# Performance work log

Hardware: AMD Instinct MI355X
Metric: run time of the kernel (lower is better)

The kernel has to match this reference:

```python
import jax, jax.numpy as jnp
import numpy as np

INDIM = 1024
OUTDIM = 2048
BATCH = 8192


def _kaiming_uniform(key, shape):
    # torch kaiming_uniform_ default: a=sqrt(5) -> gain=sqrt(2/(1+5))=sqrt(1/3),
    # fan_in = shape[0] (first dim for 2D), bound = gain*sqrt(3/fan_in) = 1/sqrt(fan_in)
    fan_in = shape[0]
    bound = 1.0 / np.sqrt(fan_in)
    return jax.random.uniform(key, shape, dtype=jnp.float32, minval=-bound, maxval=bound)


def setup_inputs() -> dict:
    key = jax.random.key(0)
    kx, kp = jax.random.split(key)
    x = jax.random.normal(kx, (BATCH, INDIM), dtype=jnp.float32)
    prototypes = _kaiming_uniform(kp, (INDIM, OUTDIM))
    return {"x": x, "prototypes": prototypes}


def reference(x, prototypes):
    # score[b, o] = -sum_i (x[b,i] - P[i,o])^2
    #             = -(||x_b||^2 - 2 x_b . P_:,o + ||P_:,o||^2)
    x_sq = jnp.sum(x * x, axis=1, keepdims=True)          # [B, 1]
    p_sq = jnp.sum(prototypes * prototypes, axis=0)       # [O]
    cross = jnp.matmul(x, prototypes)                      # [B, O] GEMM
    return 2.0 * cross - x_sq - p_sq[None, :]
```

## Files before the change

### kernel.cpp

```cpp
#include <hip/hip_runtime.h>
#include <hip/hip_bf16.h>
#include <cstdint>

#define BATCH  8192
#define INDIM  1024
#define OUTDIM 2048

typedef float  f32x4   __attribute__((ext_vector_type(4)));
typedef float  f32x16  __attribute__((ext_vector_type(16)));
typedef int    i32x2   __attribute__((ext_vector_type(2)));
typedef int    i32x4   __attribute__((ext_vector_type(4)));
typedef int    i32x8   __attribute__((ext_vector_type(8)));

__device__ __forceinline__ uint32_t pk_fp8x4(float a, float b, float c, float d) {
    uint32_t v = 0;
    v = __builtin_amdgcn_cvt_pk_fp8_f32(a, b, v, false);
    v = __builtin_amdgcn_cvt_pk_fp8_f32(c, d, v, true);
    return v;
}

__device__ __forceinline__ void async_copy16(const void* g, void* l) {
    __builtin_amdgcn_global_load_lds(
        (__attribute__((address_space(1))) void*)(g),
        (__attribute__((address_space(3))) void*)(l),
        16, 0, 0);
}

__device__ __forceinline__ int k4(int r) { return (r ^ (r >> 2)) & 3; }

__global__ __launch_bounds__(256) void prep_x(const float* __restrict__ x,
                                              uint8_t* __restrict__ xq8,
                                              float* __restrict__ xsq) {
    const int wave = threadIdx.x >> 6;
    const int lane = threadIdx.x & 63;
    const int row  = blockIdx.x * 4 + wave;
    const f32x4* src = (const f32x4*)(x + (size_t)row * INDIM);
    uint32_t* dst = (uint32_t*)(xq8 + (size_t)row * INDIM);
    float s = 0.f;
#pragma unroll
    for (int w = 0; w < 4; ++w) {
        const f32x4 v = src[lane + w * 64];
        s += v.x * v.x + v.y * v.y + v.z * v.z + v.w * v.w;
        dst[lane + w * 64] = pk_fp8x4(v.x, v.y, v.z, v.w);
    }
#pragma unroll
    for (int off = 32; off > 0; off >>= 1) s += __shfl_down(s, off);
    if (lane == 0) xsq[row] = s;
}

__global__ __launch_bounds__(256) void prep_p(const float* __restrict__ P,
                                              uint8_t* __restrict__ pt8,
                                              float* __restrict__ psq_part) {
    __shared__ float tile[64][33];
    __shared__ float psums[32];
    const int tid = threadIdx.x;
    const int o0  = blockIdx.x * 32;
    const int k0  = blockIdx.y * 256;
    const int kk  = tid >> 3;
    const int oq  = tid & 7;
    const int so  = tid >> 3;
    const int skc = (tid & 7) * 8;
    float a4[4] = {0.f, 0.f, 0.f, 0.f};
    if (tid < 32) psums[tid] = 0.f;
    for (int st = 0; st < 4; ++st) {
        __syncthreads();
#pragma unroll
        for (int r2 = 0; r2 < 2; ++r2) {
            const int k = r2 * 32 + kk;
            const float4 v = *(const float4*)(P + (size_t)(k0 + st * 64 + k) * OUTDIM + o0 + oq * 4);
            tile[k][oq * 4 + 0] = v.x;
            tile[k][oq * 4 + 1] = v.y;
            tile[k][oq * 4 + 2] = v.z;
            tile[k][oq * 4 + 3] = v.w;
            a4[0] += v.x * v.x; a4[1] += v.y * v.y;
            a4[2] += v.z * v.z; a4[3] += v.w * v.w;
        }
        __syncthreads();
        i32x2 w;
        w.x = pk_fp8x4(tile[skc + 0][so] * 32.f, tile[skc + 1][so] * 32.f,
                       tile[skc + 2][so] * 32.f, tile[skc + 3][so] * 32.f);
        w.y = pk_fp8x4(tile[skc + 4][so] * 32.f, tile[skc + 5][so] * 32.f,
                       tile[skc + 6][so] * 32.f, tile[skc + 7][so] * 32.f);
        *(i32x2*)(pt8 + (size_t)(o0 + so) * INDIM + k0 + st * 64 + skc) = w;
    }
#pragma unroll
    for (int e = 0; e < 4; ++e) atomicAdd(&psums[oq * 4 + e], a4[e]);
    __syncthreads();
    if (tid < 32) psq_part[(size_t)blockIdx.y * OUTDIM + o0 + tid] = psums[tid];
}

#define TM 256
#define TN 256
#define BKB 64

__global__ __launch_bounds__(512, 2) void gemm_ep(const uint8_t* __restrict__ xq8,
                                                  const uint8_t* __restrict__ pt8,
                                                  const float* __restrict__ xsq,
                                                  const float* __restrict__ psq_part,
                                                  float* __restrict__ out) {
    __shared__ __align__(16) uint8_t As[2][TM * BKB];
    __shared__ __align__(16) uint8_t Bs[2][TN * BKB];

    const int tid  = threadIdx.x;
    const int nb   = blockIdx.x & 7;
    const int mb   = blockIdx.x >> 3;
    const int m0   = mb * TM;
    const int n0   = nb * TN;
    const int wave = tid >> 6;
    const int lane = tid & 63;
    const int wm   = (wave >> 2) * 128;
    const int wn   = (wave & 3) * 64;
    const int l31  = lane & 31;
    const int half = lane >> 5;

    const int sr0 = tid >> 2;
    const int sq0 = (tid & 3) ^ k4(sr0);
    const int sr1 = sr0 + 128;
    const int sq1 = (tid & 3) ^ k4(sr1);

    f32x16 acc[4][2];
#pragma unroll
    for (int i = 0; i < 4; ++i)
#pragma unroll
        for (int j = 0; j < 2; ++j)
#pragma unroll
            for (int e = 0; e < 16; ++e) acc[i][j][e] = 0.f;

    async_copy16(xq8 + (size_t)(m0 + sr0) * INDIM + sq0 * 16, &As[0][tid * 16]);
    async_copy16(pt8 + (size_t)(n0 + sr0) * INDIM + sq0 * 16, &Bs[0][tid * 16]);
    async_copy16(xq8 + (size_t)(m0 + sr1) * INDIM + sq1 * 16, &As[0][(512 + tid) * 16]);
    async_copy16(pt8 + (size_t)(n0 + sr1) * INDIM + sq1 * 16, &Bs[0][(512 + tid) * 16]);
    __syncthreads();

    int cur = 0;
    for (int kb = 0; kb < INDIM; kb += BKB) {
        if (kb + BKB < INDIM) {
            const int nxt = cur ^ 1;
            const int kn  = kb + BKB;
            async_copy16(xq8 + (size_t)(m0 + sr0) * INDIM + kn + sq0 * 16, &As[nxt][tid * 16]);
            async_copy16(pt8 + (size_t)(n0 + sr0) * INDIM + kn + sq0 * 16, &Bs[nxt][tid * 16]);
            async_copy16(xq8 + (size_t)(m0 + sr1) * INDIM + kn + sq1 * 16, &As[nxt][(512 + tid) * 16]);
            async_copy16(pt8 + (size_t)(n0 + sr1) * INDIM + kn + sq1 * 16, &Bs[nxt][(512 + tid) * 16]);
        }

        i32x8 av[4], bv[2];
#pragma unroll
        for (int i = 0; i < 4; ++i) {
            const int r = wm + i * 32 + l31;
            const uint8_t* base = &As[cur][r * BKB];
            const i32x4 lo = *(const i32x4*)(base + (((half << 1) | 0) ^ k4(r)) * 16);
            const i32x4 hi = *(const i32x4*)(base + (((half << 1) | 1) ^ k4(r)) * 16);
            av[i] = __builtin_shufflevector(lo, hi, 0, 1, 2, 3, 4, 5, 6, 7);
        }
#pragma unroll
        for (int j = 0; j < 2; ++j) {
            const int r = wn + j * 32 + l31;
            const uint8_t* base = &Bs[cur][r * BKB];
            const i32x4 lo = *(const i32x4*)(base + (((half << 1) | 0) ^ k4(r)) * 16);
            const i32x4 hi = *(const i32x4*)(base + (((half << 1) | 1) ^ k4(r)) * 16);
            bv[j] = __builtin_shufflevector(lo, hi, 0, 1, 2, 3, 4, 5, 6, 7);
        }
#pragma unroll
        for (int i = 0; i < 4; ++i)
#pragma unroll
            for (int j = 0; j < 2; ++j)
                acc[i][j] = __builtin_amdgcn_mfma_scale_f32_32x32x64_f8f6f4(
                    av[i], bv[j], acc[i][j],
                    0 , 0 ,
                    0, 0x7F7F7F7F ,
                    0, 0x7F7F7F7F );

        __syncthreads();
        cur ^= 1;
    }

    const float* xsq_w = xsq + m0 + wm;
    float ps[2];
#pragma unroll
    for (int j = 0; j < 2; ++j) {
        const int n = n0 + wn + j * 32 + l31;
        ps[j] = psq_part[n] + psq_part[OUTDIM + n] +
                psq_part[2 * OUTDIM + n] + psq_part[3 * OUTDIM + n];
    }
#pragma unroll
    for (int i = 0; i < 4; ++i) {
#pragma unroll
        for (int rg = 0; rg < 16; ++rg) {
            const int rloc = (rg & 3) + 8 * (rg >> 2) + 4 * half;
            const float xs = xsq_w[i * 32 + rloc];
            float* orow = out + (size_t)(m0 + wm + i * 32 + rloc) * OUTDIM + n0 + wn + l31;
#pragma unroll
            for (int j = 0; j < 2; ++j)
                orow[j * 32] = 0.0625f * acc[i][j][rg] - xs - ps[j];
        }
    }
}

__global__ void fallback_kernel(const float* __restrict__ x,
                                const float* __restrict__ P,
                                float* __restrict__ out) {
    const int o = blockIdx.x * blockDim.x + threadIdx.x;
    const int b = blockIdx.y;
    float cr = 0.f, xq = 0.f, pq = 0.f;
    for (int i = 0; i < INDIM; ++i) {
        const float xv = x[(size_t)b * INDIM + i];
        const float pv = P[(size_t)i * OUTDIM + o];
        cr += xv * pv; xq += xv * xv; pq += pv * pv;
    }
    out[(size_t)b * OUTDIM + o] = 2.f * cr - xq - pq;
}

extern "C" void kernel_launch(void* const* d_in, const int* in_sizes, int n_in,
                              void* d_out, int out_size, void* d_ws, size_t ws_size,
                              hipStream_t stream) {
    (void)in_sizes; (void)n_in; (void)out_size;
    const float* x = (const float*)d_in[0];
    const float* P = (const float*)d_in[1];
    float* out = (float*)d_out;

    const size_t xq_bytes  = (size_t)BATCH * INDIM;
    const size_t pt_bytes  = (size_t)OUTDIM * INDIM;
    const size_t xsq_bytes = (size_t)BATCH * 4;
    const size_t psq_bytes = (size_t)4 * OUTDIM * 4;
    const size_t need = xq_bytes + pt_bytes + xsq_bytes + psq_bytes;

    if (ws_size < need) {
        fallback_kernel<<<dim3(OUTDIM / 256, BATCH), 256, 0, stream>>>(x, P, out);
        return;
    }

    uint8_t* xq8      = (uint8_t*)d_ws;
    uint8_t* pt8      = (uint8_t*)d_ws + xq_bytes;
    float*   xsq      = (float*)((char*)d_ws + xq_bytes + pt_bytes);
    float*   psq_part = xsq + BATCH;

    prep_x<<<BATCH / 4, 256, 0, stream>>>(x, xq8, xsq);
    prep_p<<<dim3(OUTDIM / 32, INDIM / 256), 256, 0, stream>>>(P, pt8, psq_part);
    gemm_ep<<<(BATCH / TM) * (OUTDIM / TN), 512, 0, stream>>>(xq8, pt8, xsq, psq_part, out);
}
```

Measured before the change: 117.8 us.

## Fuse prep kernels and load B operand directly from global into registers

Merges the x and P preprocessing kernels into one launch, with block index ranges selecting the role, to remove one kernel launch and its tail. In the GEMM, the B tile is no longer staged through shared memory. Each wave instead loads its B fragments straight from global memory into registers, prefetched one k-step ahead. This halves LDS use and cuts LDS reads, but B data is now loaded redundantly by the two M-waves, so there are more global/L2 loads per block.

```diff
diff --git a/kernel.cpp b/kernel.cpp
--- a/kernel.cpp
+++ b/kernel.cpp
@@ -28,38 +28,43 @@
 
 __device__ __forceinline__ int k4(int r) { return (r ^ (r >> 2)) & 3; }
 
-__global__ __launch_bounds__(256) void prep_x(const float* __restrict__ x,
-                                              uint8_t* __restrict__ xq8,
-                                              float* __restrict__ xsq) {
-    const int wave = threadIdx.x >> 6;
-    const int lane = threadIdx.x & 63;
-    const int row  = blockIdx.x * 4 + wave;
-    const f32x4* src = (const f32x4*)(x + (size_t)row * INDIM);
-    uint32_t* dst = (uint32_t*)(xq8 + (size_t)row * INDIM);
-    float s = 0.f;
-#pragma unroll
-    for (int w = 0; w < 4; ++w) {
-        const f32x4 v = src[lane + w * 64];
-        s += v.x * v.x + v.y * v.y + v.z * v.z + v.w * v.w;
-        dst[lane + w * 64] = pk_fp8x4(v.x, v.y, v.z, v.w);
-    }
-#pragma unroll
-    for (int off = 32; off > 0; off >>= 1) s += __shfl_down(s, off);
-    if (lane == 0) xsq[row] = s;
-}
-
-__global__ __launch_bounds__(256) void prep_p(const float* __restrict__ P,
-                                              uint8_t* __restrict__ pt8,
-                                              float* __restrict__ psq_part) {
+__global__ __launch_bounds__(256) void prep_fused(const float* __restrict__ x,
+                                                  const float* __restrict__ P,
+                                                  uint8_t* __restrict__ xq8,
+                                                  float* __restrict__ xsq,
+                                                  uint8_t* __restrict__ pt8,
+                                                  float* __restrict__ psq_part) {
     __shared__ float tile[64][33];
     __shared__ float psums[32];
     const int tid = threadIdx.x;
-    const int o0  = blockIdx.x * 32;
-    const int k0  = blockIdx.y * 256;
-    const int kk  = tid >> 3;
-    const int oq  = tid & 7;
-    const int so  = tid >> 3;
-    const int skc = (tid & 7) * 8;
+
+    if (blockIdx.x < BATCH / 4) {
+        const int wave = tid >> 6;
+        const int lane = tid & 63;
+        const int row  = blockIdx.x * 4 + wave;
+        const f32x4* src = (const f32x4*)(x + (size_t)row * INDIM);
+        uint32_t* dst = (uint32_t*)(xq8 + (size_t)row * INDIM);
+        float s = 0.f;
+#pragma unroll
+        for (int w = 0; w < 4; ++w) {
+            const f32x4 v = src[lane + w * 64];
+            s += v.x * v.x + v.y * v.y + v.z * v.z + v.w * v.w;
+            dst[lane + w * 64] = pk_fp8x4(v.x, v.y, v.z, v.w);
+        }
+#pragma unroll
+        for (int off = 32; off > 0; off >>= 1) s += __shfl_down(s, off);
+        if (lane == 0) xsq[row] = s;
+        return;
+    }
+
+    const int bx   = blockIdx.x - BATCH / 4;
+    const int o0   = (bx & 63) * 32;
+    const int kblk = bx >> 6;
+    const int k0   = kblk * 256;
+    const int kk   = tid >> 3;
+    const int oq   = tid & 7;
+    const int so   = tid >> 3;
+    const int skc  = (tid & 7) * 8;
     float a4[4] = {0.f, 0.f, 0.f, 0.f};
     if (tid < 32) psums[tid] = 0.f;
     for (int st = 0; st < 4; ++st) {
@@ -86,7 +91,7 @@
 #pragma unroll
     for (int e = 0; e < 4; ++e) atomicAdd(&psums[oq * 4 + e], a4[e]);
     __syncthreads();
-    if (tid < 32) psq_part[(size_t)blockIdx.y * OUTDIM + o0 + tid] = psums[tid];
+    if (tid < 32) psq_part[(size_t)kblk * OUTDIM + o0 + tid] = psums[tid];
 }
 
 #define TM 256
@@ -99,7 +104,6 @@
                                                   const float* __restrict__ psq_part,
                                                   float* __restrict__ out) {
     __shared__ __align__(16) uint8_t As[2][TM * BKB];
-    __shared__ __align__(16) uint8_t Bs[2][TN * BKB];
 
     const int tid  = threadIdx.x;
     const int nb   = blockIdx.x & 7;
@@ -118,6 +122,9 @@
     const int sr1 = sr0 + 128;
     const int sq1 = (tid & 3) ^ k4(sr1);
 
+    const uint8_t* bp0 = pt8 + (size_t)(n0 + wn + l31) * INDIM + half * 32;
+    const uint8_t* bp1 = pt8 + (size_t)(n0 + wn + 32 + l31) * INDIM + half * 32;
+
     f32x16 acc[4][2];
 #pragma unroll
     for (int i = 0; i < 4; ++i)
@@ -127,23 +134,36 @@
             for (int e = 0; e < 16; ++e) acc[i][j][e] = 0.f;
 
     async_copy16(xq8 + (size_t)(m0 + sr0) * INDIM + sq0 * 16, &As[0][tid * 16]);
-    async_copy16(pt8 + (size_t)(n0 + sr0) * INDIM + sq0 * 16, &Bs[0][tid * 16]);
     async_copy16(xq8 + (size_t)(m0 + sr1) * INDIM + sq1 * 16, &As[0][(512 + tid) * 16]);
-    async_copy16(pt8 + (size_t)(n0 + sr1) * INDIM + sq1 * 16, &Bs[0][(512 + tid) * 16]);
+    i32x8 bv[2];
+    {
+        const i32x4 l0 = *(const i32x4*)(bp0);
+        const i32x4 h0 = *(const i32x4*)(bp0 + 16);
+        bv[0] = __builtin_shufflevector(l0, h0, 0, 1, 2, 3, 4, 5, 6, 7);
+        const i32x4 l1 = *(const i32x4*)(bp1);
+        const i32x4 h1 = *(const i32x4*)(bp1 + 16);
+        bv[1] = __builtin_shufflevector(l1, h1, 0, 1, 2, 3, 4, 5, 6, 7);
+    }
     __syncthreads();
 
     int cur = 0;
     for (int kb = 0; kb < INDIM; kb += BKB) {
-        if (kb + BKB < INDIM) {
+        const bool more = (kb + BKB < INDIM);
+        i32x8 bvn[2];
+        if (more) {
             const int nxt = cur ^ 1;
             const int kn  = kb + BKB;
             async_copy16(xq8 + (size_t)(m0 + sr0) * INDIM + kn + sq0 * 16, &As[nxt][tid * 16]);
-            async_copy16(pt8 + (size_t)(n0 + sr0) * INDIM + kn + sq0 * 16, &Bs[nxt][tid * 16]);
             async_copy16(xq8 + (size_t)(m0 + sr1) * INDIM + kn + sq1 * 16, &As[nxt][(512 + tid) * 16]);
-            async_copy16(pt8 + (size_t)(n0 + sr1) * INDIM + kn + sq1 * 16, &Bs[nxt][(512 + tid) * 16]);
-        }
-
-        i32x8 av[4], bv[2];
+            const i32x4 l0 = *(const i32x4*)(bp0 + kn);
+            const i32x4 h0 = *(const i32x4*)(bp0 + kn + 16);
+            bvn[0] = __builtin_shufflevector(l0, h0, 0, 1, 2, 3, 4, 5, 6, 7);
+            const i32x4 l1 = *(const i32x4*)(bp1 + kn);
+            const i32x4 h1 = *(const i32x4*)(bp1 + kn + 16);
+            bvn[1] = __builtin_shufflevector(l1, h1, 0, 1, 2, 3, 4, 5, 6, 7);
+        }
+
+        i32x8 av[4];
 #pragma unroll
         for (int i = 0; i < 4; ++i) {
             const int r = wm + i * 32 + l31;
@@ -153,14 +173,6 @@
             av[i] = __builtin_shufflevector(lo, hi, 0, 1, 2, 3, 4, 5, 6, 7);
         }
 #pragma unroll
-        for (int j = 0; j < 2; ++j) {
-            const int r = wn + j * 32 + l31;
-            const uint8_t* base = &Bs[cur][r * BKB];
-            const i32x4 lo = *(const i32x4*)(base + (((half << 1) | 0) ^ k4(r)) * 16);
-            const i32x4 hi = *(const i32x4*)(base + (((half << 1) | 1) ^ k4(r)) * 16);
-            bv[j] = __builtin_shufflevector(lo, hi, 0, 1, 2, 3, 4, 5, 6, 7);
-        }
-#pragma unroll
         for (int i = 0; i < 4; ++i)
 #pragma unroll
             for (int j = 0; j < 2; ++j)
@@ -171,6 +183,7 @@
                     0, 0x7F7F7F7F );
 
         __syncthreads();
+        if (more) { bv[0] = bvn[0]; bv[1] = bvn[1]; }
         cur ^= 1;
     }
 
@@ -234,7 +247,7 @@
     float*   xsq      = (float*)((char*)d_ws + xq_bytes + pt_bytes);
     float*   psq_part = xsq + BATCH;
 
-    prep_x<<<BATCH / 4, 256, 0, stream>>>(x, xq8, xsq);
-    prep_p<<<dim3(OUTDIM / 32, INDIM / 256), 256, 0, stream>>>(P, pt8, psq_part);
+    prep_fused<<<BATCH / 4 + (OUTDIM / 32) * (INDIM / 256), 256, 0, stream>>>(
+        x, P, xq8, xsq, pt8, psq_part);
     gemm_ep<<<(BATCH / TM) * (OUTDIM / TN), 512, 0, stream>>>(xq8, pt8, xsq, psq_part, out);
 }
```

Result: slower. 128.6 us (+9.2%).
